# Kernel optimization log

Measured on AMD Instinct MI355X. Metric: run time of the kernel, lower is better.

Reference implementation:

```python
import jax, jax.numpy as jnp
import numpy as np
import math

B, C, F, W, NH = 2, 8, 1024, 512, 8
HD = F // NH


def conv2d(x, w, b):
    # NCHW 3x3 same-padding conv with bias
    y = jax.lax.conv_general_dilated(x, w, (1, 1), [(1, 1), (1, 1)],
                                     dimension_numbers=('NCHW', 'OIHW', 'NCHW'))
    return y + b[None, :, None, None]


def mc_linear(x, w):
    # per-channel linear over the feature (h) axis: (b,c,h,w) x (c,f,h) -> (b,c,f,w)
    return jnp.einsum('bchw,cfh->bcfw', x, w)


def split_heads(t):
    # (b,c,f,w) -> transpose(2,3) -> (b,c,w,f) -> (b,c,w,nh,hd) -> (b,c,nh,w,hd)
    b, c, f, w = t.shape
    return jnp.transpose(t.transpose(0, 1, 3, 2).reshape(b, c, w, NH, HD), (0, 1, 3, 2, 4))


def rotate_queries_or_keys(x):
    # lucidrains-style interleaved rotary over the sequence axis (dim -2)
    d, w = x.shape[-1], x.shape[-2]
    inv_freq = 1.0 / (10000.0 ** (jnp.arange(0, d, 2, dtype=jnp.float32) / d))
    freqs = jnp.arange(w, dtype=jnp.float32)[:, None] * inv_freq[None, :]  # (w, d/2)
    freqs = jnp.repeat(freqs, 2, axis=-1)  # (w, d)
    cos, sin = jnp.cos(freqs), jnp.sin(freqs)
    xp = x.reshape(*x.shape[:-1], d // 2, 2)
    x1, x2 = xp[..., 0], xp[..., 1]
    x_rot = jnp.stack((-x2, x1), axis=-1).reshape(x.shape)
    return x * cos + x_rot * sin


def _forward(x, prev_qk, wq_conv, bq_conv, wq_lin, wk_conv, bk_conv, wk_lin,
             wv_conv, bv_conv, wv_lin, wo_lin):
    b, c, h, w = x.shape
    q = rotate_queries_or_keys(split_heads(mc_linear(conv2d(x, wq_conv, bq_conv), wq_lin)))
    k = rotate_queries_or_keys(split_heads(mc_linear(conv2d(x, wk_conv, bk_conv), wk_lin)))
    v = split_heads(mc_linear(conv2d(x, wv_conv, bv_conv), wv_lin))
    # NOTE: original scales by sqrt(h) == sqrt(features), not sqrt(head_dim)
    qk = jnp.einsum('bcnqd,bcnkd->bcnqk', q, k) / math.sqrt(h) + prev_qk
    a = jnp.einsum('bcnqk,bcnkd->bcnqd', jax.nn.softmax(qk, axis=-1), v)
    a = jnp.transpose(a, (0, 1, 3, 2, 4)).reshape(b, c, w, h).transpose(0, 1, 3, 2)
    out = mc_linear(a, wo_lin)
    return out, qk


def setup_inputs() -> dict:
    key = jax.random.key(0)
    ks = jax.random.split(key, 10)
    s = 0.02
    return {
        'x': jax.random.normal(ks[0], (B, C, F, W), dtype=jnp.float32),
        'prev_qk': jax.random.normal(ks[1], (B, C, NH, W, W), dtype=jnp.float32) * 0.1,
        'wq_conv': jax.random.normal(ks[2], (C, C, 3, 3), dtype=jnp.float32) * s,
        'bq_conv': jnp.zeros((C,), dtype=jnp.float32),
        'wq_lin': jax.random.normal(ks[3], (C, F, F), dtype=jnp.float32) * s,
        'wk_conv': jax.random.normal(ks[4], (C, C, 3, 3), dtype=jnp.float32) * s,
        'bk_conv': jnp.zeros((C,), dtype=jnp.float32),
        'wk_lin': jax.random.normal(ks[5], (C, F, F), dtype=jnp.float32) * s,
        'wv_conv': jax.random.normal(ks[6], (C, C, 3, 3), dtype=jnp.float32) * s,
        'bv_conv': jnp.zeros((C,), dtype=jnp.float32),
        'wv_lin': jax.random.normal(ks[7], (C, F, F), dtype=jnp.float32) * s,
        'wo_lin': jax.random.normal(ks[8], (C, F, F), dtype=jnp.float32) * s,
    }


def reference(x, prev_qk, wq_conv, bq_conv, wq_lin, wk_conv, bk_conv, wk_lin,
              wv_conv, bv_conv, wv_lin, wo_lin):
    return _forward(x, prev_qk, wq_conv, bq_conv, wq_lin, wk_conv, bk_conv, wk_lin,
                    wv_conv, bv_conv, wv_lin, wo_lin)
```

## Files before the change

kernel.cpp:

```cpp
#include <hip/hip_runtime.h>
#include <stdint.h>


typedef float f32x4 __attribute__((ext_vector_type(4)));
typedef short s16x8 __attribute__((ext_vector_type(8)));

__device__ __forceinline__ short f2bf(float f) {
  union { float f; uint32_t u; } v; v.f = f;
  uint32_t r = v.u + 0x7FFFu + ((v.u >> 16) & 1u);
  return (short)(r >> 16);
}

__device__ __forceinline__ void g2l16(const void* g, void* l) {
  __builtin_amdgcn_global_load_lds(
      (const __attribute__((address_space(1))) void*)g,
      (__attribute__((address_space(3))) void*)l, 16, 0, 0);
}

template <bool AF32, bool BF32>
__device__ __forceinline__ void gemm_core(const void* __restrict__ Ap,
                                          const void* __restrict__ Bp,
                                          int K, short* sA, short* sB,
                                          f32x4 (*acc)[4]) {
  const int tid = threadIdx.x;
  const int lane = tid & 63;
  const int wv = tid >> 6;
  const int wm = wv >> 1, wn = wv & 1;
  const int q = lane >> 4, cix = lane & 15;

  for (int k0 = 0; k0 < K; k0 += 32) {
    __syncthreads();
    if constexpr (!BF32) {
      const short* Bs = (const short*)Bp;
#pragma unroll
      for (int i = 0; i < 2; ++i) {
        int seg = wv + 4 * i;
        int m = seg * 16 + (lane >> 2);
        int ko = (lane & 3) * 8;
        g2l16(Bs + (size_t)m * K + k0 + ko, sB + seg * 512);
      }
    } else {
      const float* Bf = (const float*)Bp;
      int m = tid >> 1, ho = (tid & 1) * 16;
      const float* src = Bf + (size_t)m * K + k0 + ho;
      float4 v0 = *(const float4*)(src);
      float4 v1 = *(const float4*)(src + 4);
      float4 v2 = *(const float4*)(src + 8);
      float4 v3 = *(const float4*)(src + 12);
      s16x8 o0, o1;
      o0[0]=f2bf(v0.x); o0[1]=f2bf(v0.y); o0[2]=f2bf(v0.z); o0[3]=f2bf(v0.w);
      o0[4]=f2bf(v1.x); o0[5]=f2bf(v1.y); o0[6]=f2bf(v1.z); o0[7]=f2bf(v1.w);
      o1[0]=f2bf(v2.x); o1[1]=f2bf(v2.y); o1[2]=f2bf(v2.z); o1[3]=f2bf(v2.w);
      o1[4]=f2bf(v3.x); o1[5]=f2bf(v3.y); o1[6]=f2bf(v3.z); o1[7]=f2bf(v3.w);
      *(s16x8*)(sB + m * 32 + ho) = o0;
      *(s16x8*)(sB + m * 32 + ho + 8) = o1;
    }
    if constexpr (!AF32) {
      const short* As = (const short*)Ap;
#pragma unroll
      for (int i = 0; i < 2; ++i) {
        int seg = wv + 4 * i;
        int m = seg * 16 + (lane >> 2);
        int ko = (lane & 3) * 8;
        g2l16(As + (size_t)m * K + k0 + ko, sA + seg * 512);
      }
    } else {
      const float* Af = (const float*)Ap;
      int m = tid >> 1, ho = (tid & 1) * 16;
      const float* src = Af + (size_t)m * K + k0 + ho;
      float4 v0 = *(const float4*)(src);
      float4 v1 = *(const float4*)(src + 4);
      float4 v2 = *(const float4*)(src + 8);
      float4 v3 = *(const float4*)(src + 12);
      s16x8 o0, o1;
      o0[0]=f2bf(v0.x); o0[1]=f2bf(v0.y); o0[2]=f2bf(v0.z); o0[3]=f2bf(v0.w);
      o0[4]=f2bf(v1.x); o0[5]=f2bf(v1.y); o0[6]=f2bf(v1.z); o0[7]=f2bf(v1.w);
      o1[0]=f2bf(v2.x); o1[1]=f2bf(v2.y); o1[2]=f2bf(v2.z); o1[3]=f2bf(v2.w);
      o1[4]=f2bf(v3.x); o1[5]=f2bf(v3.y); o1[6]=f2bf(v3.z); o1[7]=f2bf(v3.w);
      *(s16x8*)(sA + m * 32 + ho) = o0;
      *(s16x8*)(sA + m * 32 + ho + 8) = o1;
    }
    __syncthreads();
    s16x8 afr[4], bfr[4];
#pragma unroll
    for (int i = 0; i < 4; ++i)
      afr[i] = *(const s16x8*)(sA + (wm * 64 + i * 16 + cix) * 32 + q * 8);
#pragma unroll
    for (int i = 0; i < 4; ++i)
      bfr[i] = *(const s16x8*)(sB + (wn * 64 + i * 16 + cix) * 32 + q * 8);
#pragma unroll
    for (int i = 0; i < 4; ++i)
#pragma unroll
      for (int j = 0; j < 4; ++j)
        acc[i][j] = __builtin_amdgcn_mfma_f32_16x16x32_bf16(afr[i], bfr[j],
                                                            acc[i][j], 0, 0, 0);
  }
}

__global__ void __launch_bounds__(256) k_conv(
    const float* __restrict__ x,
    const float* __restrict__ wqc, const float* __restrict__ bqc,
    const float* __restrict__ wkc, const float* __restrict__ bkc,
    const float* __restrict__ wvc, const float* __restrict__ bvc,
    short* __restrict__ Yt) {
  __shared__ float xs[8][66][19];
  const int h0 = blockIdx.x * 64, w0 = blockIdx.y * 16, b = blockIdx.z;
  const int tid = threadIdx.x;
  for (int idx = tid; idx < 8 * 66 * 18; idx += 256) {
    int c = idx / (66 * 18);
    int rem = idx % (66 * 18);
    int r = rem / 18, cc = rem % 18;
    int h = h0 + r - 1, w = w0 + cc - 1;
    float v = 0.f;
    if (h >= 0 && h < 1024 && w >= 0 && w < 512)
      v = x[(((size_t)b * 8 + c) << 10 | (unsigned)h) * 512 + w];
    xs[c][r][cc] = v;
  }
  __syncthreads();
  const int hh = tid & 63;
  const int wv4 = tid >> 6;
  float aq[4][8], ak[4][8], av[4][8];
#pragma unroll
  for (int jj = 0; jj < 4; ++jj)
#pragma unroll
    for (int co = 0; co < 8; ++co) {
      aq[jj][co] = bqc[co]; ak[jj][co] = bkc[co]; av[jj][co] = bvc[co];
    }
  for (int ci = 0; ci < 8; ++ci)
#pragma unroll
    for (int dh = 0; dh < 3; ++dh)
#pragma unroll
      for (int dw = 0; dw < 3; ++dw) {
        float xv[4];
#pragma unroll
        for (int jj = 0; jj < 4; ++jj) xv[jj] = xs[ci][hh + dh][wv4 * 4 + jj + dw];
        const int wi = ci * 9 + dh * 3 + dw;
#pragma unroll
        for (int co = 0; co < 8; ++co) {
          float wq_ = wqc[co * 72 + wi];
          float wk_ = wkc[co * 72 + wi];
          float wv_ = wvc[co * 72 + wi];
#pragma unroll
          for (int jj = 0; jj < 4; ++jj) {
            aq[jj][co] = fmaf(xv[jj], wq_, aq[jj][co]);
            ak[jj][co] = fmaf(xv[jj], wk_, ak[jj][co]);
            av[jj][co] = fmaf(xv[jj], wv_, av[jj][co]);
          }
        }
      }
  const size_t hgl = h0 + hh;
#pragma unroll
  for (int jj = 0; jj < 4; ++jj) {
    size_t col = (size_t)b * 512 + w0 + wv4 * 4 + jj;
#pragma unroll
    for (int co = 0; co < 8; ++co) {
      Yt[((size_t)co << 20) + (col << 10) + hgl] = f2bf(aq[jj][co]);
      Yt[((size_t)(8 + co) << 20) + (col << 10) + hgl] = f2bf(ak[jj][co]);
      Yt[((size_t)(16 + co) << 20) + (col << 10) + hgl] = f2bf(av[jj][co]);
    }
  }
}

__global__ void __launch_bounds__(256) k_qkv(
    const float* __restrict__ wql, const float* __restrict__ wkl,
    const float* __restrict__ wvl, const short* __restrict__ Yt,
    short* __restrict__ Qr, short* __restrict__ Kr, short* __restrict__ Vt) {
  __shared__ short sA[128 * 32], sB[128 * 32];
  const int by = blockIdx.y;
  const int proj = by >> 3, cq = by & 7;
  const int mt = blockIdx.x >> 3, nt = blockIdx.x & 7;
  const float* wl = (proj == 0) ? wql : ((proj == 1) ? wkl : wvl);
  const float* A = wl + ((size_t)cq << 20) + ((size_t)mt << 17);
  const short* B = Yt + ((size_t)by << 20) + ((size_t)nt << 17);
  const f32x4 fzero = {0.f, 0.f, 0.f, 0.f};
  f32x4 acc[4][4];
#pragma unroll
  for (int i = 0; i < 4; ++i)
#pragma unroll
    for (int j = 0; j < 4; ++j) acc[i][j] = fzero;
  gemm_core<true, false>(A, B, 1024, sA, sB, acc);

  const int lane = threadIdx.x & 63, wv = threadIdx.x >> 6;
  const int wm = wv >> 1, wn = wv & 1, q = lane >> 4, cix = lane & 15;
  const int head = mt;
  if (proj == 2) {
#pragma unroll
    for (int mi = 0; mi < 4; ++mi) {
      int rbase = wm * 64 + mi * 16 + q * 4;
#pragma unroll
      for (int ni = 0; ni < 4; ++ni) {
        int col = nt * 128 + wn * 64 + ni * 16 + cix;
        int b = col >> 9, wpos = col & 511;
        size_t base = ((size_t)((cq * 8 + head) * 2 + b) << 16) +
                      ((size_t)rbase << 9) + wpos;
        f32x4 v = acc[mi][ni];
        Vt[base] = f2bf(v[0]);
        Vt[base + 512] = f2bf(v[1]);
        Vt[base + 1024] = f2bf(v[2]);
        Vt[base + 1536] = f2bf(v[3]);
      }
    }
  } else {
    short* QKp = proj ? Kr : Qr;
#pragma unroll
    for (int mi = 0; mi < 4; ++mi) {
      int rbase = wm * 64 + mi * 16 + q * 4;
      int j0 = rbase >> 1;
      float if0 = exp2f(-0.20762050593046f * (float)j0);
      float if1 = exp2f(-0.20762050593046f * (float)(j0 + 1));
#pragma unroll
      for (int ni = 0; ni < 4; ++ni) {
        int col = nt * 128 + wn * 64 + ni * 16 + cix;
        int b = col >> 9, wpos = col & 511;
        float fw = (float)wpos;
        float s0, c0, s1, c1;
        __sincosf(fw * if0, &s0, &c0);
        __sincosf(fw * if1, &s1, &c1);
        f32x4 v = acc[mi][ni];
        short4 pk;
        pk.x = f2bf(v[0] * c0 - v[1] * s0);
        pk.y = f2bf(v[1] * c0 + v[0] * s0);
        pk.z = f2bf(v[2] * c1 - v[3] * s1);
        pk.w = f2bf(v[3] * c1 + v[2] * s1);
        *(short4*)&QKp[((size_t)(((cq * 8 + head) * 2 + b) * 512 + wpos) << 7) +
                       rbase] = pk;
      }
    }
  }
}

__global__ void __launch_bounds__(256) k_s(
    const short* __restrict__ Qr, const short* __restrict__ Kr,
    const float* __restrict__ prevqk, float* __restrict__ qk,
    float* __restrict__ Pm, float* __restrict__ Pl) {
  __shared__ short sA[128 * 32], sB[128 * 32];
  __shared__ float smax[128][2], ssum[128][2];
  const int tid = threadIdx.x, lane = tid & 63, wv = tid >> 6;
  const int wm = wv >> 1, wn = wv & 1, q = lane >> 4, cix = lane & 15;
  const int qt = blockIdx.x >> 2, kt = blockIdx.x & 3;
  const int bcn = blockIdx.y;
  const size_t qbase = ((size_t)bcn) << 16;
  const int b = bcn >> 6, cch = (bcn >> 3) & 7, nh = bcn & 7;
  const size_t qrb = ((size_t)((cch * 8 + nh) * 2 + b)) << 16;
  (void)qbase;
  const short* A = Qr + qrb + ((size_t)qt << 14);
  const short* B = Kr + qrb + ((size_t)kt << 14);
  const f32x4 fzero = {0.f, 0.f, 0.f, 0.f};
  f32x4 acc[4][4];
#pragma unroll
  for (int i = 0; i < 4; ++i)
#pragma unroll
    for (int j = 0; j < 4; ++j) acc[i][j] = fzero;
  gemm_core<false, false>(A, B, 128, sA, sB, acc);

  const size_t rowg0 = (size_t)bcn * 512 + qt * 128;
#pragma unroll
  for (int mi = 0; mi < 4; ++mi) {
#pragma unroll
    for (int ni = 0; ni < 4; ++ni) {
      int rl = wm * 64 + mi * 16 + q * 4;
      int cl = kt * 128 + wn * 64 + ni * 16 + cix;
      size_t base = ((rowg0 + rl) << 9) + cl;
#pragma unroll
      for (int r = 0; r < 4; ++r) {
        float s = acc[mi][ni][r] * 0.03125f + prevqk[base + (size_t)r * 512];
        qk[base + (size_t)r * 512] = s;
        acc[mi][ni][r] = s;
      }
    }
  }
#pragma unroll
  for (int mi = 0; mi < 4; ++mi) {
#pragma unroll
    for (int r = 0; r < 4; ++r) {
      float m = fmaxf(fmaxf(acc[mi][0][r], acc[mi][1][r]),
                      fmaxf(acc[mi][2][r], acc[mi][3][r]));
      m = fmaxf(m, __shfl_xor(m, 1));
      m = fmaxf(m, __shfl_xor(m, 2));
      m = fmaxf(m, __shfl_xor(m, 4));
      m = fmaxf(m, __shfl_xor(m, 8));
      float se = __expf(acc[mi][0][r] - m) + __expf(acc[mi][1][r] - m) +
                 __expf(acc[mi][2][r] - m) + __expf(acc[mi][3][r] - m);
      se += __shfl_xor(se, 1);
      se += __shfl_xor(se, 2);
      se += __shfl_xor(se, 4);
      se += __shfl_xor(se, 8);
      if (cix == 0) {
        int row = wm * 64 + mi * 16 + q * 4 + r;
        smax[row][wn] = m;
        ssum[row][wn] = se;
      }
    }
  }
  __syncthreads();
  if (tid < 128) {
    float m0 = smax[tid][0], m1 = smax[tid][1];
    float M = fmaxf(m0, m1);
    float S = ssum[tid][0] * __expf(m0 - M) + ssum[tid][1] * __expf(m1 - M);
    Pm[(rowg0 + tid) * 4 + kt] = M;
    Pl[(rowg0 + tid) * 4 + kt] = S;
  }
}

__global__ void __launch_bounds__(256) k_pv(
    const float* __restrict__ qk, const short* __restrict__ Vt,
    const float* __restrict__ Pm, const float* __restrict__ Pl,
    short* __restrict__ At) {
  __shared__ short Pt[128 * 136];
  __shared__ float rowM[128], rowL[128];
  const int tid = threadIdx.x, lane = tid & 63, wv = tid >> 6;
  const int wm = wv >> 1, wn = wv & 1, q = lane >> 4, cix = lane & 15;
  const int qt = blockIdx.x, bcn = blockIdx.y;
  const int b = bcn >> 6, cch = (bcn >> 3) & 7, nh = bcn & 7;
  const size_t rowg0 = (size_t)bcn * 512 + qt * 128;
  if (tid < 128) {
    size_t ridx = (rowg0 + tid) * 4;
    float m0 = Pm[ridx], m1 = Pm[ridx + 1], m2 = Pm[ridx + 2], m3 = Pm[ridx + 3];
    float M = fmaxf(fmaxf(m0, m1), fmaxf(m2, m3));
    float L = Pl[ridx] * __expf(m0 - M) + Pl[ridx + 1] * __expf(m1 - M) +
              Pl[ridx + 2] * __expf(m2 - M) + Pl[ridx + 3] * __expf(m3 - M);
    rowM[tid] = M;
    rowL[tid] = 1.0f / L;
  }
  __syncthreads();
  const f32x4 fzero = {0.f, 0.f, 0.f, 0.f};
  f32x4 acc[4][4];
#pragma unroll
  for (int i = 0; i < 4; ++i)
#pragma unroll
    for (int j = 0; j < 4; ++j) acc[i][j] = fzero;
  const size_t vbase = ((size_t)((cch * 8 + nh) * 2 + b)) << 16;

  for (int kt2 = 0; kt2 < 4; ++kt2) {
    __syncthreads();
#pragma unroll
    for (int i = 0; i < 16; ++i) {
      int chunk = tid + 256 * i;
      int r = chunk >> 5, co = (chunk & 31) * 4;
      float4 sv = *(const float4*)&qk[((rowg0 + r) << 9) + kt2 * 128 + co];
      float M = rowM[r], iL = rowL[r];
      short4 p;
      p.x = f2bf(__expf(sv.x - M) * iL);
      p.y = f2bf(__expf(sv.y - M) * iL);
      p.z = f2bf(__expf(sv.z - M) * iL);
      p.w = f2bf(__expf(sv.w - M) * iL);
      *(short4*)&Pt[r * 136 + co] = p;
    }
    __syncthreads();
#pragma unroll
    for (int s = 0; s < 4; ++s) {
      s16x8 afr[4], bfr[4];
#pragma unroll
      for (int i = 0; i < 4; ++i)
        afr[i] = *(const s16x8*)&Pt[(wm * 64 + i * 16 + cix) * 136 + s * 32 + q * 8];
#pragma unroll
      for (int i = 0; i < 4; ++i)
        bfr[i] = *(const s16x8*)&Vt[vbase + ((size_t)(wn * 64 + i * 16 + cix) << 9) +
                                    kt2 * 128 + s * 32 + q * 8];
#pragma unroll
      for (int i = 0; i < 4; ++i)
#pragma unroll
        for (int j = 0; j < 4; ++j)
          acc[i][j] = __builtin_amdgcn_mfma_f32_16x16x32_bf16(afr[i], bfr[j],
                                                              acc[i][j], 0, 0, 0);
    }
  }
#pragma unroll
  for (int mi = 0; mi < 4; ++mi) {
    int wq = qt * 128 + wm * 64 + mi * 16 + q * 4;
#pragma unroll
    for (int ni = 0; ni < 4; ++ni) {
      int dl = wn * 64 + ni * 16 + cix;
      size_t ob = (((size_t)cch << 10) + b * 512 + wq) * 1024 + nh * 128 + dl;
      f32x4 v = acc[mi][ni];
      At[ob] = f2bf(v[0]);
      At[ob + 1024] = f2bf(v[1]);
      At[ob + 2048] = f2bf(v[2]);
      At[ob + 3072] = f2bf(v[3]);
    }
  }
}

__global__ void __launch_bounds__(256) k_out(
    const short* __restrict__ At, const float* __restrict__ wol,
    float* __restrict__ outp) {
  __shared__ short sA[128 * 32], sB[128 * 32];
  const int c = blockIdx.y;
  const int mt = blockIdx.x >> 3, nt = blockIdx.x & 7;
  const short* A = At + ((size_t)c << 20) + ((size_t)mt << 17);
  const float* B = wol + ((size_t)c << 20) + ((size_t)nt << 17);
  const f32x4 fzero = {0.f, 0.f, 0.f, 0.f};
  f32x4 acc[4][4];
#pragma unroll
  for (int i = 0; i < 4; ++i)
#pragma unroll
    for (int j = 0; j < 4; ++j) acc[i][j] = fzero;
  gemm_core<false, true>(A, B, 1024, sA, sB, acc);

  const int lane = threadIdx.x & 63, wv = threadIdx.x >> 6;
  const int wm = wv >> 1, wn = wv & 1, q = lane >> 4, cix = lane & 15;
#pragma unroll
  for (int mi = 0; mi < 4; ++mi) {
    int colm = mt * 128 + wm * 64 + mi * 16 + q * 4;
    int b = colm >> 9, w = colm & 511;
#pragma unroll
    for (int ni = 0; ni < 4; ++ni) {
      int f = nt * 128 + wn * 64 + ni * 16 + cix;
      f32x4 v = acc[mi][ni];
      float4 st; st.x = v[0]; st.y = v[1]; st.z = v[2]; st.w = v[3];
      *(float4*)&outp[((((size_t)b * 8 + c) << 10) + f) * 512 + w] = st;
    }
  }
}

extern "C" void kernel_launch(void* const* d_in, const int* in_sizes, int n_in,
                              void* d_out, int out_size, void* d_ws,
                              size_t ws_size, hipStream_t stream) {
  const float* x = (const float*)d_in[0];
  const float* prevqk = (const float*)d_in[1];
  const float* wqc = (const float*)d_in[2];
  const float* bqc = (const float*)d_in[3];
  const float* wql = (const float*)d_in[4];
  const float* wkc = (const float*)d_in[5];
  const float* bkc = (const float*)d_in[6];
  const float* wkl = (const float*)d_in[7];
  const float* wvc = (const float*)d_in[8];
  const float* bvc = (const float*)d_in[9];
  const float* wvl = (const float*)d_in[10];
  const float* wol = (const float*)d_in[11];
  float* outp = (float*)d_out;
  float* qk = outp + 8388608;

  char* ws = (char*)d_ws;
  short* Yt = (short*)ws;
  short* Qr = (short*)(ws + 50331648);
  short* Kr = (short*)(ws + 67108864);
  short* Vt = (short*)(ws + 83886080);
  float* Pm = (float*)(ws + 100663296);
  float* Pl = (float*)(ws + 101711872);
  short* At = (short*)ws;

  k_conv<<<dim3(16, 32, 2), 256, 0, stream>>>(x, wqc, bqc, wkc, bkc, wvc, bvc, Yt);
  k_qkv<<<dim3(64, 24), 256, 0, stream>>>(wql, wkl, wvl, Yt, Qr, Kr, Vt);
  k_s<<<dim3(16, 128), 256, 0, stream>>>(Qr, Kr, prevqk, qk, Pm, Pl);
  k_pv<<<dim3(4, 128), 256, 0, stream>>>(qk, Vt, Pm, Pl, At);
  k_out<<<dim3(64, 8), 256, 0, stream>>>(At, wol, outp);
}
```

Measured before the change: 705.3 us.

## Pre-convert linear weights to bf16 and remap GEMM block order

```diff
diff --git a/kernel.cpp b/kernel.cpp
--- a/kernel.cpp
+++ b/kernel.cpp
@@ -17,9 +17,8 @@
       (__attribute__((address_space(3))) void*)l, 16, 0, 0);
 }
 
-template <bool AF32, bool BF32>
-__device__ __forceinline__ void gemm_core(const void* __restrict__ Ap,
-                                          const void* __restrict__ Bp,
+__device__ __forceinline__ void gemm_core(const short* __restrict__ A,
+                                          const short* __restrict__ B,
                                           int K, short* sA, short* sB,
                                           f32x4 (*acc)[4]) {
   const int tid = threadIdx.x;
@@ -30,55 +29,19 @@
 
   for (int k0 = 0; k0 < K; k0 += 32) {
     __syncthreads();
-    if constexpr (!BF32) {
-      const short* Bs = (const short*)Bp;
-#pragma unroll
-      for (int i = 0; i < 2; ++i) {
-        int seg = wv + 4 * i;
-        int m = seg * 16 + (lane >> 2);
-        int ko = (lane & 3) * 8;
-        g2l16(Bs + (size_t)m * K + k0 + ko, sB + seg * 512);
-      }
-    } else {
-      const float* Bf = (const float*)Bp;
-      int m = tid >> 1, ho = (tid & 1) * 16;
-      const float* src = Bf + (size_t)m * K + k0 + ho;
-      float4 v0 = *(const float4*)(src);
-      float4 v1 = *(const float4*)(src + 4);
-      float4 v2 = *(const float4*)(src + 8);
-      float4 v3 = *(const float4*)(src + 12);
-      s16x8 o0, o1;
-      o0[0]=f2bf(v0.x); o0[1]=f2bf(v0.y); o0[2]=f2bf(v0.z); o0[3]=f2bf(v0.w);
-      o0[4]=f2bf(v1.x); o0[5]=f2bf(v1.y); o0[6]=f2bf(v1.z); o0[7]=f2bf(v1.w);
-      o1[0]=f2bf(v2.x); o1[1]=f2bf(v2.y); o1[2]=f2bf(v2.z); o1[3]=f2bf(v2.w);
-      o1[4]=f2bf(v3.x); o1[5]=f2bf(v3.y); o1[6]=f2bf(v3.z); o1[7]=f2bf(v3.w);
-      *(s16x8*)(sB + m * 32 + ho) = o0;
-      *(s16x8*)(sB + m * 32 + ho + 8) = o1;
-    }
-    if constexpr (!AF32) {
-      const short* As = (const short*)Ap;
-#pragma unroll
-      for (int i = 0; i < 2; ++i) {
-        int seg = wv + 4 * i;
-        int m = seg * 16 + (lane >> 2);
-        int ko = (lane & 3) * 8;
-        g2l16(As + (size_t)m * K + k0 + ko, sA + seg * 512);
-      }
-    } else {
-      const float* Af = (const float*)Ap;
-      int m = tid >> 1, ho = (tid & 1) * 16;
-      const float* src = Af + (size_t)m * K + k0 + ho;
-      float4 v0 = *(const float4*)(src);
-      float4 v1 = *(const float4*)(src + 4);
-      float4 v2 = *(const float4*)(src + 8);
-      float4 v3 = *(const float4*)(src + 12);
-      s16x8 o0, o1;
-      o0[0]=f2bf(v0.x); o0[1]=f2bf(v0.y); o0[2]=f2bf(v0.z); o0[3]=f2bf(v0.w);
-      o0[4]=f2bf(v1.x); o0[5]=f2bf(v1.y); o0[6]=f2bf(v1.z); o0[7]=f2bf(v1.w);
-      o1[0]=f2bf(v2.x); o1[1]=f2bf(v2.y); o1[2]=f2bf(v2.z); o1[3]=f2bf(v2.w);
-      o1[4]=f2bf(v3.x); o1[5]=f2bf(v3.y); o1[6]=f2bf(v3.z); o1[7]=f2bf(v3.w);
-      *(s16x8*)(sA + m * 32 + ho) = o0;
-      *(s16x8*)(sA + m * 32 + ho + 8) = o1;
+#pragma unroll
+    for (int i = 0; i < 2; ++i) {
+      int seg = wv + 4 * i;
+      int m = seg * 16 + (lane >> 2);
+      int ko = (lane & 3) * 8;
+      g2l16(B + (size_t)m * K + k0 + ko, sB + seg * 512);
+    }
+#pragma unroll
+    for (int i = 0; i < 2; ++i) {
+      int seg = wv + 4 * i;
+      int m = seg * 16 + (lane >> 2);
+      int ko = (lane & 3) * 8;
+      g2l16(A + (size_t)m * K + k0 + ko, sA + seg * 512);
     }
     __syncthreads();
     s16x8 afr[4], bfr[4];
@@ -94,6 +57,22 @@
       for (int j = 0; j < 4; ++j)
         acc[i][j] = __builtin_amdgcn_mfma_f32_16x16x32_bf16(afr[i], bfr[j],
                                                             acc[i][j], 0, 0, 0);
+  }
+}
+
+__global__ void __launch_bounds__(256) k_cvt(
+    const float* __restrict__ w0, const float* __restrict__ w1,
+    const float* __restrict__ w2, const float* __restrict__ w3,
+    short* __restrict__ Wb) {
+  size_t i = (size_t)blockIdx.x * 256 + threadIdx.x;
+#pragma unroll
+  for (int r = 0; r < 4; ++r) {
+    const float* s = (r == 0) ? w0 : (r == 1) ? w1 : (r == 2) ? w2 : w3;
+    size_t v = i + (size_t)r * 2097152;
+    float4 f = *(const float4*)(s + (i << 2));
+    short4 o;
+    o.x = f2bf(f.x); o.y = f2bf(f.y); o.z = f2bf(f.z); o.w = f2bf(f.w);
+    *(short4*)(Wb + (v << 2)) = o;
   }
 }
 
@@ -162,23 +141,24 @@
 }
 
 __global__ void __launch_bounds__(256) k_qkv(
-    const float* __restrict__ wql, const float* __restrict__ wkl,
-    const float* __restrict__ wvl, const short* __restrict__ Yt,
+    const short* __restrict__ Wb, const short* __restrict__ Yt,
     short* __restrict__ Qr, short* __restrict__ Kr, short* __restrict__ Vt) {
   __shared__ short sA[128 * 32], sB[128 * 32];
-  const int by = blockIdx.y;
-  const int proj = by >> 3, cq = by & 7;
-  const int mt = blockIdx.x >> 3, nt = blockIdx.x & 7;
-  const float* wl = (proj == 0) ? wql : ((proj == 1) ? wkl : wvl);
-  const float* A = wl + ((size_t)cq << 20) + ((size_t)mt << 17);
-  const short* B = Yt + ((size_t)by << 20) + ((size_t)nt << 17);
+  const int L = blockIdx.x;
+  const int lin = (L & 7) * 192 + (L >> 3);
+  const int g = lin >> 6;
+  const int t = lin & 63;
+  const int proj = g >> 3, cq = g & 7;
+  const int mt = t >> 3, nt = t & 7;
+  const short* A = Wb + ((size_t)g << 20) + ((size_t)mt << 17);
+  const short* B = Yt + ((size_t)g << 20) + ((size_t)nt << 17);
   const f32x4 fzero = {0.f, 0.f, 0.f, 0.f};
   f32x4 acc[4][4];
 #pragma unroll
   for (int i = 0; i < 4; ++i)
 #pragma unroll
     for (int j = 0; j < 4; ++j) acc[i][j] = fzero;
-  gemm_core<true, false>(A, B, 1024, sA, sB, acc);
+  gemm_core(A, B, 1024, sA, sB, acc);
 
   const int lane = threadIdx.x & 63, wv = threadIdx.x >> 6;
   const int wm = wv >> 1, wn = wv & 1, q = lane >> 4, cix = lane & 15;
@@ -239,10 +219,8 @@
   const int wm = wv >> 1, wn = wv & 1, q = lane >> 4, cix = lane & 15;
   const int qt = blockIdx.x >> 2, kt = blockIdx.x & 3;
   const int bcn = blockIdx.y;
-  const size_t qbase = ((size_t)bcn) << 16;
   const int b = bcn >> 6, cch = (bcn >> 3) & 7, nh = bcn & 7;
   const size_t qrb = ((size_t)((cch * 8 + nh) * 2 + b)) << 16;
-  (void)qbase;
   const short* A = Qr + qrb + ((size_t)qt << 14);
   const short* B = Kr + qrb + ((size_t)kt << 14);
   const f32x4 fzero = {0.f, 0.f, 0.f, 0.f};
@@ -251,7 +229,7 @@
   for (int i = 0; i < 4; ++i)
 #pragma unroll
     for (int j = 0; j < 4; ++j) acc[i][j] = fzero;
-  gemm_core<false, false>(A, B, 128, sA, sB, acc);
+  gemm_core(A, B, 128, sA, sB, acc);
 
   const size_t rowg0 = (size_t)bcn * 512 + qt * 128;
 #pragma unroll
@@ -382,20 +360,23 @@
 }
 
 __global__ void __launch_bounds__(256) k_out(
-    const short* __restrict__ At, const float* __restrict__ wol,
+    const short* __restrict__ At, const short* __restrict__ Wob,
     float* __restrict__ outp) {
   __shared__ short sA[128 * 32], sB[128 * 32];
-  const int c = blockIdx.y;
-  const int mt = blockIdx.x >> 3, nt = blockIdx.x & 7;
+  const int L = blockIdx.x;
+  const int lin = (L & 7) * 64 + (L >> 3);
+  const int c = lin >> 6;
+  const int t = lin & 63;
+  const int mt = t >> 3, nt = t & 7;
   const short* A = At + ((size_t)c << 20) + ((size_t)mt << 17);
-  const float* B = wol + ((size_t)c << 20) + ((size_t)nt << 17);
+  const short* B = Wob + ((size_t)c << 20) + ((size_t)nt << 17);
   const f32x4 fzero = {0.f, 0.f, 0.f, 0.f};
   f32x4 acc[4][4];
 #pragma unroll
   for (int i = 0; i < 4; ++i)
 #pragma unroll
     for (int j = 0; j < 4; ++j) acc[i][j] = fzero;
-  gemm_core<false, true>(A, B, 1024, sA, sB, acc);
+  gemm_core(A, B, 1024, sA, sB, acc);
 
   const int lane = threadIdx.x & 63, wv = threadIdx.x >> 6;
   const int wm = wv >> 1, wn = wv & 1, q = lane >> 4, cix = lane & 15;
@@ -432,17 +413,20 @@
   float* qk = outp + 8388608;
 
   char* ws = (char*)d_ws;
-  short* Yt = (short*)ws;
-  short* Qr = (short*)(ws + 50331648);
-  short* Kr = (short*)(ws + 67108864);
-  short* Vt = (short*)(ws + 83886080);
-  float* Pm = (float*)(ws + 100663296);
-  float* Pl = (float*)(ws + 101711872);
-  short* At = (short*)ws;
-
+  short* Wb = (short*)ws;
+  short* Yt = (short*)(ws + 67108864);
+  short* Qr = (short*)(ws + 117440512);
+  short* Kr = (short*)(ws + 134217728);
+  short* Vt = (short*)(ws + 150994944);
+  float* Pm = (float*)(ws + 167772160);
+  float* Pl = (float*)(ws + 168820736);
+  short* At = (short*)(ws + 67108864);
+  short* Wob = Wb + ((size_t)24 << 20);
+
+  k_cvt<<<dim3(8192), 256, 0, stream>>>(wql, wkl, wvl, wol, Wb);
   k_conv<<<dim3(16, 32, 2), 256, 0, stream>>>(x, wqc, bqc, wkc, bkc, wvc, bvc, Yt);
-  k_qkv<<<dim3(64, 24), 256, 0, stream>>>(wql, wkl, wvl, Yt, Qr, Kr, Vt);
+  k_qkv<<<dim3(1536), 256, 0, stream>>>(Wb, Yt, Qr, Kr, Vt);
   k_s<<<dim3(16, 128), 256, 0, stream>>>(Qr, Kr, prevqk, qk, Pm, Pl);
   k_pv<<<dim3(4, 128), 256, 0, stream>>>(qk, Vt, Pm, Pl, At);
-  k_out<<<dim3(64, 8), 256, 0, stream>>>(At, wol, outp);
-}
+  k_out<<<dim3(512), 256, 0, stream>>>(At, Wob, outp);
+}
```

Result: faster. 678.7 us (-3.8%).
